# Kernel optimization log

Hardware: AMD Instinct MI355X
Metric: run time of the kernel (lower is better)

The kernel has to match this reference:

```python
import jax, jax.numpy as jnp
import numpy as np

G, N, F_IN, H, C = 128, 512, 128, 128, 10
LAMB = 1.0
NEG_SLOPE = 0.2
P_EDGE = 32.0 / N  # avg degree ~32


def setup_inputs() -> dict:
    key = jax.random.key(0)
    ks = jax.random.split(key, 12)
    x = jax.random.normal(ks[0], (G, N, F_IN), dtype=jnp.float32)
    # symmetric 0/1 adjacency without self loops (per-graph dense block)
    a = (jax.random.uniform(ks[1], (G, N, N)) < P_EDGE).astype(jnp.float32)
    adj = jnp.maximum(a, jnp.swapaxes(a, 1, 2)) * (1.0 - jnp.eye(N, dtype=jnp.float32))

    def lin(k, fi, fo):
        return (jax.random.normal(k, (fi, fo), dtype=jnp.float32) / np.float32(np.sqrt(fi)))

    return {
        "x": x, "adj": adj,
        "W1": lin(ks[2], F_IN, H), "b1": jnp.zeros((H,), jnp.float32),
        "W2": lin(ks[3], H, H), "b2": jnp.zeros((H,), jnp.float32),
        "W3": lin(ks[4], H, H), "b3": jnp.zeros((H,), jnp.float32),
        "att1_s": 0.1 * jax.random.normal(ks[5], (H,), dtype=jnp.float32),
        "att1_d": 0.1 * jax.random.normal(ks[6], (H,), dtype=jnp.float32),
        "att2_s": 0.1 * jax.random.normal(ks[7], (H,), dtype=jnp.float32),
        "att2_d": 0.1 * jax.random.normal(ks[8], (H,), dtype=jnp.float32),
        "Wl1": lin(ks[9], 2 * H, H), "bl1": jnp.zeros((H,), jnp.float32),
        "Wl2": lin(ks[10], H, H // 2), "bl2": jnp.zeros((H // 2,), jnp.float32),
        "Wl3": lin(ks[11], H // 2, C), "bl3": jnp.zeros((C,), jnp.float32),
    }


def gcn(x, adj, W, b):
    # GCNConv: D^{-1/2} (A + I) D^{-1/2} X W + b  (self-loop weight 1, edge weights in adj)
    deg = adj.sum(-1) + 1.0                              # [G, n]
    dinv = jax.lax.rsqrt(deg)
    xw = x @ W                                           # [G, n, H]
    agg = jnp.einsum('gij,gjf->gif', adj, dinv[..., None] * xw)
    return dinv[..., None] * agg + (dinv * dinv)[..., None] * xw + b


def info_score(x, adj):
    # HGP-SL node information score: row-wise L1 norm of (I - D^{-1} A) X
    deg = jnp.maximum(adj.sum(-1), 1.0)
    agg = jnp.einsum('gij,gjf->gif', adj, x) / deg[..., None]
    return jnp.sum(jnp.abs(x - agg), axis=-1)            # [G, n]


def hgpsl_pool(x, adj, att_s, att_d, k):
    # top-k node selection by information score, then structure learning:
    # dense (sample=False) path: e_ij = leaky_relu(att.[x_i||x_j]) + lamb*A_ij, softmax over j
    s = info_score(x, adj)
    _, idx = jax.lax.top_k(s, k)                         # [G, k]
    xk = jnp.take_along_axis(x, idx[..., None], axis=1)  # [G, k, H]
    g = jnp.arange(x.shape[0])[:, None, None]
    ak = adj[g, idx[:, :, None], idx[:, None, :]]        # induced adjacency [G, k, k]
    e = jax.nn.leaky_relu((xk @ att_s)[:, :, None] + (xk @ att_d)[:, None, :], NEG_SLOPE)
    attn = jax.nn.softmax(e + LAMB * ak, axis=-1)        # new learned edge weights
    return xk, attn


def readout(x):
    # gmp || gap over nodes
    return jnp.concatenate([x.max(axis=1), x.mean(axis=1)], axis=-1)


def reference(x, adj, W1, b1, W2, b2, W3, b3, att1_s, att1_d, att2_s, att2_d,
              Wl1, bl1, Wl2, bl2, Wl3, bl3):
    h = jax.nn.relu(gcn(x, adj, W1, b1))
    h, a1 = hgpsl_pool(h, adj, att1_s, att1_d, N // 2)
    x1 = readout(h)
    h = jax.nn.relu(gcn(h, a1, W2, b2))
    h, a2 = hgpsl_pool(h, a1, att2_s, att2_d, N // 4)
    x2 = readout(h)
    h = jax.nn.relu(gcn(h, a2, W3, b3))
    x3 = readout(h)
    z = jax.nn.relu(x1) + jax.nn.relu(x2) + jax.nn.relu(x3)
    z = jax.nn.relu(z @ Wl1 + bl1)
    z = jax.nn.relu(z @ Wl2 + bl2)
    return jax.nn.softmax(z @ Wl3 + bl3, axis=-1)
```

## Files before the change

### kernel.cpp

```cpp
#include <hip/hip_runtime.h>

#define Gg   128
#define N1   512
#define FH   128
#define K1   256
#define K2   128

typedef __bf16 bf16x8 __attribute__((ext_vector_type(8)));
typedef float  floatx4 __attribute__((ext_vector_type(4)));

__device__ inline float wredsum(float v) {
#pragma unroll
    for (int o = 32; o; o >>= 1) v += __shfl_xor(v, o, 64);
    return v;
}
__device__ inline float wredmax(float v) {
#pragma unroll
    for (int o = 32; o; o >>= 1) v = fmaxf(v, __shfl_xor(v, o, 64));
    return v;
}
__device__ inline unsigned short bf_rne(float x) {
    unsigned u = __float_as_uint(x);
    return (unsigned short)((u + 0x7fffu + ((u >> 16) & 1u)) >> 16);
}
__device__ __forceinline__ void gll16(const void* gsrc, void* lds) {
    __builtin_amdgcn_global_load_lds(
        (const __attribute__((address_space(1))) unsigned int*)gsrc,
        (__attribute__((address_space(3))) unsigned int*)lds, 16, 0, 0);
}

__global__ __launch_bounds__(256) void k_prep(const float* __restrict__ adj,
        float* __restrict__ dinv_gcn, float* __restrict__ dinv_info) {
    int wave = threadIdx.x >> 6, lane = threadIdx.x & 63;
    long long row = (long long)blockIdx.x * 4 + wave;
    const float* ar = adj + row * N1;
    float s = 0.f;
#pragma unroll
    for (int c = 0; c < 2; ++c) {
        float4 v = *(const float4*)(ar + lane * 8 + c * 4);
        s += (v.x + v.y) + (v.z + v.w);
    }
    s = wredsum(s);
    if (lane == 0) {
        dinv_gcn[row]  = rsqrtf(s + 1.0f);
        dinv_info[row] = 1.0f / fmaxf(s, 1.0f);
    }
}

__global__ __launch_bounds__(256) void k_tsplit(const float* __restrict__ feat,
        unsigned short* __restrict__ Thi, unsigned short* __restrict__ Tmid,
        unsigned short* __restrict__ Tlo) {
    __shared__ float tile[64 * 65];
    int b = blockIdx.x;
    int g = b >> 4, rb = (b >> 1) & 7, cb = b & 1;
    int t = threadIdx.x;
    {
        int r0 = t >> 4, c4 = t & 15;
#pragma unroll
        for (int i = 0; i < 4; ++i) {
            int r = r0 + i * 16;
            float4 v = *(const float4*)(feat + ((long long)g * 512 + rb * 64 + r) * 128 + cb * 64 + c4 * 4);
            tile[r * 65 + c4 * 4 + 0] = v.x;
            tile[r * 65 + c4 * 4 + 1] = v.y;
            tile[r * 65 + c4 * 4 + 2] = v.z;
            tile[r * 65 + c4 * 4 + 3] = v.w;
        }
    }
    __syncthreads();
    int tf = t >> 2, chunk = t & 3;
    unsigned short hbuf[16] __attribute__((aligned(16)));
    unsigned short mbuf[16] __attribute__((aligned(16)));
    unsigned short lbuf[16] __attribute__((aligned(16)));
#pragma unroll
    for (int i = 0; i < 16; ++i) {
        int m = chunk * 16 + i;
        float v = tile[m * 65 + tf];
        unsigned short h = bf_rne(v);
        float fh = __uint_as_float((unsigned)h << 16);
        float r1 = v - fh;
        unsigned short md = bf_rne(r1);
        float fm = __uint_as_float((unsigned)md << 16);
        float r2 = r1 - fm;
        unsigned short lo = bf_rne(r2);
        hbuf[i] = h; mbuf[i] = md; lbuf[i] = lo;
    }
    int f = cb * 64 + tf;
    long long obase = (long long)g * 65536 + (rb * 2 + (chunk >> 1)) * 4096
                    + f * 32 + (chunk & 1) * 16;
    *(uint4*)(Thi + obase)      = *(const uint4*)&hbuf[0];
    *(uint4*)(Thi + obase + 8)  = *(const uint4*)&hbuf[8];
    *(uint4*)(Tmid + obase)     = *(const uint4*)&mbuf[0];
    *(uint4*)(Tmid + obase + 8) = *(const uint4*)&mbuf[8];
    *(uint4*)(Tlo + obase)      = *(const uint4*)&lbuf[0];
    *(uint4*)(Tlo + obase + 8)  = *(const uint4*)&lbuf[8];
}

template<int EPI>
__global__ __launch_bounds__(256) void k_aggmm(const float* __restrict__ adjf,
        const unsigned short* __restrict__ Bhi, const unsigned short* __restrict__ Bmid,
        const unsigned short* __restrict__ Blo,
        const float* __restrict__ dvec, const float* __restrict__ hx,
        const float* __restrict__ bias, float* __restrict__ outH, float* __restrict__ outS) {
    __shared__ unsigned short Al[128 * 40];
    __shared__ unsigned short Blin[3][4096];
    __shared__ float sred[2][128];
    int b = blockIdx.x;
    int g  = (b & 7) + ((b >> 5) << 3);
    int rb = (b >> 3) & 3;
    int tid = threadIdx.x;
    int w = tid >> 6, lane = tid & 63;
    int wm = w >> 1, wn = w & 1;
    int ln = lane & 15, quad = lane >> 4;
    floatx4 acc[4][4];
#pragma unroll
    for (int i = 0; i < 4; ++i)
#pragma unroll
        for (int j = 0; j < 4; ++j) { floatx4 z = {0.f, 0.f, 0.f, 0.f}; acc[i][j] = z; }

    const char* bsrc0 = (const char*)(Bhi  + (long long)g * 65536);
    const char* bsrc1 = (const char*)(Bmid + (long long)g * 65536);
    const char* bsrc2 = (const char*)(Blo  + (long long)g * 65536);
    const long long arow0 = ((long long)g * 512 + rb * 128) * 512;
    for (int kk = 0; kk < 512; kk += 32) {
        __syncthreads();
        {
            long long soff = (long long)(kk >> 5) * 8192 + (w * 2048) + (lane << 4);
            char* l0 = (char*)&Blin[0][0] + w * 2048;
            char* l1 = (char*)&Blin[1][0] + w * 2048;
            char* l2 = (char*)&Blin[2][0] + w * 2048;
            gll16(bsrc0 + soff,        l0);
            gll16(bsrc0 + soff + 1024, l0 + 1024);
            gll16(bsrc1 + soff,        l1);
            gll16(bsrc1 + soff + 1024, l1 + 1024);
            gll16(bsrc2 + soff,        l2);
            gll16(bsrc2 + soff + 1024, l2 + 1024);
        }
#pragma unroll
        for (int i = 0; i < 4; ++i) {
            int id = tid + i * 256;
            int r = id >> 3, c = id & 7;
            float4 v = *(const float4*)(adjf + arow0 + (long long)r * 512 + kk + c * 4);
            ushort4 u;
            u.x = (unsigned short)(__float_as_uint(v.x) >> 16);
            u.y = (unsigned short)(__float_as_uint(v.y) >> 16);
            u.z = (unsigned short)(__float_as_uint(v.z) >> 16);
            u.w = (unsigned short)(__float_as_uint(v.w) >> 16);
            *(ushort4*)&Al[r * 40 + c * 4] = u;
        }
        __syncthreads();
        bf16x8 af[4];
#pragma unroll
        for (int tm = 0; tm < 4; ++tm)
            af[tm] = *(const bf16x8*)&Al[(wm * 64 + tm * 16 + ln) * 40 + quad * 8];
#pragma unroll
        for (int s = 0; s < 3; ++s) {
#pragma unroll
            for (int tn = 0; tn < 4; ++tn) {
                bf16x8 bfr = *(const bf16x8*)&Blin[s][(wn * 64 + tn * 16 + ln) * 32 + quad * 8];
#pragma unroll
                for (int tm = 0; tm < 4; ++tm)
                    acc[tm][tn] = __builtin_amdgcn_mfma_f32_16x16x32_bf16(af[tm], bfr, acc[tm][tn], 0, 0, 0);
            }
        }
    }
    long long rowbase = (long long)g * 512 + rb * 128;
    if (EPI == 0) {
#pragma unroll
        for (int tm = 0; tm < 4; ++tm)
#pragma unroll
        for (int r = 0; r < 4; ++r) {
            int ml = wm * 64 + tm * 16 + quad * 4 + r;
            long long grow = rowbase + ml;
            float di = dvec[grow];
#pragma unroll
            for (int tn = 0; tn < 4; ++tn) {
                int nc = wn * 64 + tn * 16 + ln;
                float hv = hx[grow * 128 + nc];
                float o = fmaxf(fmaf(di, acc[tm][tn][r] + hv, bias[nc]), 0.f);
                outH[grow * 128 + nc] = o;
            }
        }
    } else {
#pragma unroll
        for (int tm = 0; tm < 4; ++tm)
#pragma unroll
        for (int r = 0; r < 4; ++r) {
            int ml = wm * 64 + tm * 16 + quad * 4 + r;
            long long grow = rowbase + ml;
            float di = dvec[grow];
            float v = 0.f;
#pragma unroll
            for (int tn = 0; tn < 4; ++tn) {
                int nc = wn * 64 + tn * 16 + ln;
                float hv = hx[grow * 128 + nc];
                v += fabsf(hv - acc[tm][tn][r] * di);
            }
            v += __shfl_xor(v, 1); v += __shfl_xor(v, 2);
            v += __shfl_xor(v, 4); v += __shfl_xor(v, 8);
            if (ln == 0) sred[wn][ml] = v;
        }
        __syncthreads();
        if (tid < 128) outS[rowbase + tid] = sred[0][tid] + sred[1][tid];
    }
}

__global__ __launch_bounds__(256) void k_gemm_rw(const float* __restrict__ A,
        const float* __restrict__ W, float* __restrict__ C,
        const float* __restrict__ rs) {
    __shared__ float Al[64][68];
    __shared__ float Wl[64][132];
    long long row0 = (long long)blockIdx.x * 64;
    int tid = threadIdx.x, tr = tid >> 4, tc = tid & 15;
    float acc[4][8] = {};
    for (int ch = 0; ch < 2; ++ch) {
        for (int p = tid; p < 1024; p += 256) {
            int r = p >> 4, c4 = p & 15;
            *(float4*)&Al[r][c4 * 4] = *(const float4*)(A + (row0 + r) * 128 + ch * 64 + c4 * 4);
        }
        for (int p = tid; p < 2048; p += 256) {
            int r = p >> 5, c4 = p & 31;
            *(float4*)&Wl[r][c4 * 4] = *(const float4*)(W + (ch * 64 + r) * 128 + c4 * 4);
        }
        __syncthreads();
        for (int k = 0; k < 64; ++k) {
            float4 w0 = *(const float4*)&Wl[k][tc * 8];
            float4 w1 = *(const float4*)&Wl[k][tc * 8 + 4];
            float w[8] = {w0.x, w0.y, w0.z, w0.w, w1.x, w1.y, w1.z, w1.w};
#pragma unroll
            for (int i = 0; i < 4; ++i) {
                float a = Al[tr * 4 + i][k];
#pragma unroll
                for (int j = 0; j < 8; ++j) acc[i][j] = fmaf(a, w[j], acc[i][j]);
            }
        }
        __syncthreads();
    }
#pragma unroll
    for (int i = 0; i < 4; ++i) {
        long long r = row0 + tr * 4 + i;
        float sc = rs ? rs[r] : 1.0f;
        *(float4*)(C + r * 128 + tc * 8)     = make_float4(sc * acc[i][0], sc * acc[i][1], sc * acc[i][2], sc * acc[i][3]);
        *(float4*)(C + r * 128 + tc * 8 + 4) = make_float4(sc * acc[i][4], sc * acc[i][5], sc * acc[i][6], sc * acc[i][7]);
    }
}

template<int NT, int KSEL>
__global__ __launch_bounds__(256) void k_topk(const float* __restrict__ s, int* __restrict__ idx) {
    __shared__ unsigned long long keys[NT];
    int g = blockIdx.x;
    const float* sg = s + g * NT;
    for (int t = threadIdx.x; t < NT; t += 256) {
        unsigned int b = __float_as_uint(sg[t]);
        unsigned int ord = (b & 0x80000000u) ? ~b : (b | 0x80000000u);
        keys[t] = ((unsigned long long)(~ord) << 32) | (unsigned int)t;
    }
    __syncthreads();
    for (int k = 2; k <= NT; k <<= 1) {
        for (int j = k >> 1; j > 0; j >>= 1) {
            for (int i = threadIdx.x; i < NT; i += 256) {
                int l = i ^ j;
                if (l > i) {
                    bool dir = ((i & k) == 0);
                    unsigned long long a = keys[i], b2 = keys[l];
                    bool sw = dir ? (a > b2) : (a < b2);
                    if (sw) { keys[i] = b2; keys[l] = a; }
                }
            }
            __syncthreads();
        }
    }
    for (int t = threadIdx.x; t < KSEL; t += 256)
        idx[g * KSEL + t] = (int)(keys[t] & 0xffffffffu);
}

template<int KK>
__global__ __launch_bounds__(256) void k_gather(const float* __restrict__ h, int srcN,
        const int* __restrict__ idx, const float* __restrict__ atts, const float* __restrict__ attd,
        float* __restrict__ xk, float* __restrict__ as_, float* __restrict__ ad_) {
    int wave = threadIdx.x >> 6, lane = threadIdx.x & 63;
    int r = blockIdx.x * 4 + wave;
    int g = r / KK;
    int j = idx[r];
    float2 v = *(const float2*)(h + ((long long)g * srcN + j) * 128 + lane * 2);
    *(float2*)(xk + (long long)r * 128 + lane * 2) = v;
    float2 sv = *(const float2*)(atts + lane * 2);
    float2 dv = *(const float2*)(attd + lane * 2);
    float ps = v.x * sv.x + v.y * sv.y;
    float pd = v.x * dv.x + v.y * dv.y;
    ps = wredsum(ps); pd = wredsum(pd);
    if (lane == 0) { as_[r] = ps; ad_[r] = pd; }
}

template<int KK, int SRCN>
__global__ __launch_bounds__(256) void k_attn(const float* __restrict__ adjSrc,
        const int* __restrict__ idx, const float* __restrict__ as_, const float* __restrict__ ad_,
        float* __restrict__ attn, float* __restrict__ dgo, float* __restrict__ dio) {
    constexpr int E = KK / 64;
    __shared__ int   idxL[KK];
    __shared__ float adL[KK];
    __shared__ float rowL[4][SRCN];
    int bpg = KK / 4;
    int g = blockIdx.x / bpg;
    int wave = threadIdx.x >> 6, lane = threadIdx.x & 63;
    int i = (blockIdx.x % bpg) * 4 + wave;
    for (int t = threadIdx.x; t < KK; t += 256) { idxL[t] = idx[g * KK + t]; adL[t] = ad_[g * KK + t]; }
    __syncthreads();
    int ri = idxL[i];
    const float* arow = adjSrc + ((long long)g * SRCN + ri) * SRCN;
    for (int c = lane; c < SRCN; c += 64) rowL[wave][c] = arow[c];
    float asi = as_[g * KK + i];
    float vals[E];
    float m = -1e30f;
#pragma unroll
    for (int e = 0; e < E; ++e) {
        int j = e * 64 + lane;
        float x = asi + adL[j];
        x = (x >= 0.f) ? x : 0.2f * x;
        x += rowL[wave][idxL[j]];
        vals[e] = x; m = fmaxf(m, x);
    }
    m = wredmax(m);
    float S = 0.f;
#pragma unroll
    for (int e = 0; e < E; ++e) { vals[e] = expf(vals[e] - m); S += vals[e]; }
    S = wredsum(S);
    float inv = 1.f / S, rs = 0.f;
    float* orow = attn + ((long long)g * KK + i) * KK;
#pragma unroll
    for (int e = 0; e < E; ++e) { float p = vals[e] * inv; rs += p; orow[e * 64 + lane] = p; }
    rs = wredsum(rs);
    if (lane == 0) { dgo[g * KK + i] = rsqrtf(rs + 1.f); dio[g * KK + i] = 1.f / fmaxf(rs, 1.f); }
}

template<int KK>
__global__ __launch_bounds__(128) void k_readout(const float* __restrict__ xk, float* __restrict__ xo) {
    int g = blockIdx.x, f = threadIdx.x;
    const float* p = xk + (long long)g * KK * 128 + f;
    float m = -1e30f, s = 0.f;
    for (int r = 0; r < KK; ++r) { float v = p[r * 128]; m = fmaxf(m, v); s += v; }
    xo[g * 256 + f] = m;
    xo[g * 256 + 128 + f] = s * (1.0f / KK);
}

template<int KK, bool SCALEY, int EPI>
__global__ __launch_bounds__(256) void k_agg(const float* __restrict__ A, const float* __restrict__ Y,
        const float* __restrict__ dg, const float* __restrict__ di_,
        const float* __restrict__ bias, const float* __restrict__ hx,
        float* __restrict__ outH, float* __restrict__ outS) {
    __shared__ float Al[64][68];
    __shared__ float Yl[64][132];
    __shared__ float red[64][17];
    constexpr int RB = KK / 64;
    int g = blockIdx.x / RB;
    int rb = blockIdx.x % RB;
    const float* Ag = A + (long long)g * KK * KK;
    const float* Yg = Y + (long long)g * KK * 128;
    int tid = threadIdx.x, tr = tid >> 4, tc = tid & 15;
    float acc[4][8] = {};
    for (int ch = 0; ch < KK / 64; ++ch) {
        for (int p = tid; p < 1024; p += 256) {
            int r = p >> 4, c4 = p & 15;
            *(float4*)&Al[r][c4 * 4] = *(const float4*)(Ag + (rb * 64 + r) * KK + ch * 64 + c4 * 4);
        }
        for (int p = tid; p < 2048; p += 256) {
            int r = p >> 5, c4 = p & 31;
            float4 v = *(const float4*)(Yg + (ch * 64 + r) * 128 + c4 * 4);
            if (SCALEY) { float sc = dg[g * KK + ch * 64 + r]; v.x *= sc; v.y *= sc; v.z *= sc; v.w *= sc; }
            *(float4*)&Yl[r][c4 * 4] = v;
        }
        __syncthreads();
        for (int k = 0; k < 64; ++k) {
            float4 w0 = *(const float4*)&Yl[k][tc * 8];
            float4 w1 = *(const float4*)&Yl[k][tc * 8 + 4];
            float w[8] = {w0.x, w0.y, w0.z, w0.w, w1.x, w1.y, w1.z, w1.w};
#pragma unroll
            for (int i = 0; i < 4; ++i) {
                float a = Al[tr * 4 + i][k];
#pragma unroll
                for (int j = 0; j < 8; ++j) acc[i][j] = fmaf(a, w[j], acc[i][j]);
            }
        }
        __syncthreads();
    }
    int i0 = rb * 64 + tr * 4;
    if (EPI == 0) {
#pragma unroll
        for (int i = 0; i < 4; ++i) {
            long long gi = (long long)g * KK + i0 + i;
            float d = dg[gi], dd = d * d;
            float4 x0 = *(const float4*)(hx + gi * 128 + tc * 8);
            float4 x1 = *(const float4*)(hx + gi * 128 + tc * 8 + 4);
            float4 b0 = *(const float4*)(bias + tc * 8);
            float4 b1 = *(const float4*)(bias + tc * 8 + 4);
            float4 o0, o1;
            o0.x = fmaxf(fmaf(d, acc[i][0], fmaf(dd, x0.x, b0.x)), 0.f);
            o0.y = fmaxf(fmaf(d, acc[i][1], fmaf(dd, x0.y, b0.y)), 0.f);
            o0.z = fmaxf(fmaf(d, acc[i][2], fmaf(dd, x0.z, b0.z)), 0.f);
            o0.w = fmaxf(fmaf(d, acc[i][3], fmaf(dd, x0.w, b0.w)), 0.f);
            o1.x = fmaxf(fmaf(d, acc[i][4], fmaf(dd, x1.x, b1.x)), 0.f);
            o1.y = fmaxf(fmaf(d, acc[i][5], fmaf(dd, x1.y, b1.y)), 0.f);
            o1.z = fmaxf(fmaf(d, acc[i][6], fmaf(dd, x1.z, b1.z)), 0.f);
            o1.w = fmaxf(fmaf(d, acc[i][7], fmaf(dd, x1.w, b1.w)), 0.f);
            *(float4*)(outH + gi * 128 + tc * 8)     = o0;
            *(float4*)(outH + gi * 128 + tc * 8 + 4) = o1;
        }
    } else {
#pragma unroll
        for (int i = 0; i < 4; ++i) {
            long long gi = (long long)g * KK + i0 + i;
            float d = di_[gi];
            float4 x0 = *(const float4*)(hx + gi * 128 + tc * 8);
            float4 x1 = *(const float4*)(hx + gi * 128 + tc * 8 + 4);
            float p = fabsf(x0.x - acc[i][0] * d) + fabsf(x0.y - acc[i][1] * d)
                    + fabsf(x0.z - acc[i][2] * d) + fabsf(x0.w - acc[i][3] * d)
                    + fabsf(x1.x - acc[i][4] * d) + fabsf(x1.y - acc[i][5] * d)
                    + fabsf(x1.z - acc[i][6] * d) + fabsf(x1.w - acc[i][7] * d);
            red[tr * 4 + i][tc] = p;
        }
        __syncthreads();
        if (tid < 64) {
            float s = 0.f;
#pragma unroll
            for (int t = 0; t < 16; ++t) s += red[tid][t];
            outS[(long long)g * KK + rb * 64 + tid] = s;
        }
    }
}

__global__ __launch_bounds__(128) void k_mlp(const float* __restrict__ x1, const float* __restrict__ x2,
        const float* __restrict__ x3,
        const float* __restrict__ Wl1, const float* __restrict__ bl1,
        const float* __restrict__ Wl2, const float* __restrict__ bl2,
        const float* __restrict__ Wl3, const float* __restrict__ bl3,
        float* __restrict__ out) {
    __shared__ float z[256], z1[128], z2[64], lg[10];
    int g = blockIdx.x, t = threadIdx.x;
    for (int k = t; k < 256; k += 128)
        z[k] = fmaxf(x1[g * 256 + k], 0.f) + fmaxf(x2[g * 256 + k], 0.f) + fmaxf(x3[g * 256 + k], 0.f);
    __syncthreads();
    {
        float acc = bl1[t];
        for (int k = 0; k < 256; ++k) acc = fmaf(z[k], Wl1[k * 128 + t], acc);
        z1[t] = fmaxf(acc, 0.f);
    }
    __syncthreads();
    if (t < 64) {
        float acc = bl2[t];
        for (int k = 0; k < 128; ++k) acc = fmaf(z1[k], Wl2[k * 64 + t], acc);
        z2[t] = fmaxf(acc, 0.f);
    }
    __syncthreads();
    if (t < 10) {
        float acc = bl3[t];
        for (int k = 0; k < 64; ++k) acc = fmaf(z2[k], Wl3[k * 10 + t], acc);
        lg[t] = acc;
    }
    __syncthreads();
    if (t == 0) {
        float m = -1e30f;
        for (int c = 0; c < 10; ++c) m = fmaxf(m, lg[c]);
        float S = 0.f;
        float e[10];
        for (int c = 0; c < 10; ++c) { e[c] = expf(lg[c] - m); S += e[c]; }
        float inv = 1.f / S;
        for (int c = 0; c < 10; ++c) out[g * 10 + c] = e[c] * inv;
    }
}

extern "C" void kernel_launch(void* const* d_in, const int* in_sizes, int n_in,
                              void* d_out, int out_size, void* d_ws, size_t ws_size,
                              hipStream_t stream) {
    const float* x     = (const float*)d_in[0];
    const float* adj   = (const float*)d_in[1];
    const float* W1    = (const float*)d_in[2];
    const float* b1    = (const float*)d_in[3];
    const float* W2    = (const float*)d_in[4];
    const float* b2    = (const float*)d_in[5];
    const float* W3    = (const float*)d_in[6];
    const float* b3    = (const float*)d_in[7];
    const float* att1s = (const float*)d_in[8];
    const float* att1d = (const float*)d_in[9];
    const float* att2s = (const float*)d_in[10];
    const float* att2d = (const float*)d_in[11];
    const float* Wl1   = (const float*)d_in[12];
    const float* bl1   = (const float*)d_in[13];
    const float* Wl2   = (const float*)d_in[14];
    const float* bl2   = (const float*)d_in[15];
    const float* Wl3   = (const float*)d_in[16];
    const float* bl3   = (const float*)d_in[17];
    float* out = (float*)d_out;

    char* ws = (char*)d_ws;
    unsigned short* Thi  = (unsigned short*)(ws + 0);
    unsigned short* Tmid = (unsigned short*)(ws + 16777216);
    unsigned short* Tlo  = (unsigned short*)(ws + 33554432);
    float* xk1 = (float*)(ws + 0);
    float* xw2 = (float*)(ws + 16777216);
    float* h2  = (float*)(ws + 33554432);
    float* xk2 = (float*)(ws + 16777216);
    float* a2  = (float*)(ws + 25165824);
    float* xw3 = (float*)(ws + 0);
    float* h3  = (float*)(ws + 8388608);
    float* dxw1 = (float*)(ws + 50331648);
    float* h1   = dxw1;
    float* a1   = dxw1;
    float* s1      = (float*)(ws + 83886080);
    int*   idx1    = (int*)  (ws + 84148224);
    float* as1     = (float*)(ws + 84279296);
    float* ad1     = (float*)(ws + 84410368);
    float* dinv_g1 = (float*)(ws + 84541440);
    float* dinv_i1 = (float*)(ws + 84803584);
    float* dinv_g2 = (float*)(ws + 85065728);
    float* dinv_i2 = (float*)(ws + 85196800);
    float* x1r     = (float*)(ws + 85327872);
    float* s2      = (float*)(ws + 85458944);
    int*   idx2    = (int*)  (ws + 85590016);
    float* as2     = (float*)(ws + 85655552);
    float* ad2     = (float*)(ws + 85721088);
    float* dinv_g3 = (float*)(ws + 85786624);
    float* dinv_i3 = (float*)(ws + 85852160);
    float* x2r     = (float*)(ws + 85917696);
    float* x3r     = (float*)(ws + 86048768);

    k_prep<<<Gg * N1 / 4, 256, 0, stream>>>(adj, dinv_g1, dinv_i1);
    k_gemm_rw<<<Gg * N1 / 64, 256, 0, stream>>>(x, W1, dxw1, dinv_g1);
    k_tsplit<<<Gg * 16, 256, 0, stream>>>(dxw1, Thi, Tmid, Tlo);
    k_aggmm<0><<<Gg * 4, 256, 0, stream>>>(adj, Thi, Tmid, Tlo, dinv_g1, dxw1, b1, h1, nullptr);
    k_tsplit<<<Gg * 16, 256, 0, stream>>>(h1, Thi, Tmid, Tlo);
    k_aggmm<1><<<Gg * 4, 256, 0, stream>>>(adj, Thi, Tmid, Tlo, dinv_i1, h1, nullptr, nullptr, s1);
    k_topk<N1, K1><<<Gg, 256, 0, stream>>>(s1, idx1);
    k_gather<K1><<<Gg * K1 / 4, 256, 0, stream>>>(h1, N1, idx1, att1s, att1d, xk1, as1, ad1);
    k_readout<K1><<<Gg, 128, 0, stream>>>(xk1, x1r);
    k_attn<K1, N1><<<Gg * K1 / 4, 256, 0, stream>>>(adj, idx1, as1, ad1, a1, dinv_g2, dinv_i2);

    k_gemm_rw<<<Gg * K1 / 64, 256, 0, stream>>>(xk1, W2, xw2, nullptr);
    k_agg<K1, true, 0><<<Gg * (K1 / 64), 256, 0, stream>>>(a1, xw2, dinv_g2, dinv_i2, b2, xw2, h2, nullptr);
    k_agg<K1, false, 1><<<Gg * (K1 / 64), 256, 0, stream>>>(a1, h2, dinv_g2, dinv_i2, b2, h2, nullptr, s2);
    k_topk<K1, K2><<<Gg, 256, 0, stream>>>(s2, idx2);
    k_gather<K2><<<Gg * K2 / 4, 256, 0, stream>>>(h2, K1, idx2, att2s, att2d, xk2, as2, ad2);
    k_readout<K2><<<Gg, 128, 0, stream>>>(xk2, x2r);
    k_attn<K2, K1><<<Gg * K2 / 4, 256, 0, stream>>>(a1, idx2, as2, ad2, a2, dinv_g3, dinv_i3);

    k_gemm_rw<<<Gg * K2 / 64, 256, 0, stream>>>(xk2, W3, xw3, nullptr);
    k_agg<K2, true, 0><<<Gg * (K2 / 64), 256, 0, stream>>>(a2, xw3, dinv_g3, dinv_i3, b3, xw3, h3, nullptr);
    k_readout<K2><<<Gg, 128, 0, stream>>>(h3, x3r);

    k_mlp<<<Gg, 128, 0, stream>>>(x1r, x2r, x3r, Wl1, bl1, Wl2, bl2, Wl3, bl3, out);
}
```

Baseline: 599.3 us.

## Pre-convert adjacency to bf16 once and stream it via async LDS loads with XOR swizzle

k_prep now writes a bf16 copy of the adjacency while it computes degrees. Both k_aggmm launches then read this half-size copy with global_load_lds instead of reading fp32 rows and converting them in registers. The A and B LDS tiles use an XOR-swizzled 64-byte row layout, and k_tsplit writes its output pre-swizzled to match, so fragment reads avoid bank conflicts without padding. This cuts adjacency traffic in the two big aggregation passes and removes the per-tile conversion. In exchange it adds one extra bf16 write of the full adjacency and relies on the workspace being large enough at the new offset.

Measured after the change: 607.6 us. No clear change (+1.4%).

```diff
diff --git a/kernel.cpp b/kernel.cpp
--- a/kernel.cpp
+++ b/kernel.cpp
@@ -30,16 +30,23 @@
 }
 
 __global__ __launch_bounds__(256) void k_prep(const float* __restrict__ adj,
+        unsigned short* __restrict__ adjbf,
         float* __restrict__ dinv_gcn, float* __restrict__ dinv_info) {
     int wave = threadIdx.x >> 6, lane = threadIdx.x & 63;
     long long row = (long long)blockIdx.x * 4 + wave;
     const float* ar = adj + row * N1;
     float s = 0.f;
+    unsigned short ub[8] __attribute__((aligned(16)));
 #pragma unroll
     for (int c = 0; c < 2; ++c) {
         float4 v = *(const float4*)(ar + lane * 8 + c * 4);
         s += (v.x + v.y) + (v.z + v.w);
-    }
+        ub[c * 4 + 0] = (unsigned short)(__float_as_uint(v.x) >> 16);
+        ub[c * 4 + 1] = (unsigned short)(__float_as_uint(v.y) >> 16);
+        ub[c * 4 + 2] = (unsigned short)(__float_as_uint(v.z) >> 16);
+        ub[c * 4 + 3] = (unsigned short)(__float_as_uint(v.w) >> 16);
+    }
+    *(uint4*)(adjbf + row * N1 + lane * 8) = *(const uint4*)ub;
     s = wredsum(s);
     if (lane == 0) {
         dinv_gcn[row]  = rsqrtf(s + 1.0f);
@@ -84,24 +91,26 @@
         unsigned short lo = bf_rne(r2);
         hbuf[i] = h; mbuf[i] = md; lbuf[i] = lo;
     }
-    int f = cb * 64 + tf;
+    int sxz = (tf >> 1) & 3;
+    int c0 = (chunk & 1) * 2;
+    int p0 = (c0 ^ sxz) * 8, p1 = ((c0 + 1) ^ sxz) * 8;
     long long obase = (long long)g * 65536 + (rb * 2 + (chunk >> 1)) * 4096
-                    + f * 32 + (chunk & 1) * 16;
-    *(uint4*)(Thi + obase)      = *(const uint4*)&hbuf[0];
-    *(uint4*)(Thi + obase + 8)  = *(const uint4*)&hbuf[8];
-    *(uint4*)(Tmid + obase)     = *(const uint4*)&mbuf[0];
-    *(uint4*)(Tmid + obase + 8) = *(const uint4*)&mbuf[8];
-    *(uint4*)(Tlo + obase)      = *(const uint4*)&lbuf[0];
-    *(uint4*)(Tlo + obase + 8)  = *(const uint4*)&lbuf[8];
+                    + (cb * 64 + tf) * 32;
+    *(uint4*)(Thi + obase + p0)  = *(const uint4*)&hbuf[0];
+    *(uint4*)(Thi + obase + p1)  = *(const uint4*)&hbuf[8];
+    *(uint4*)(Tmid + obase + p0) = *(const uint4*)&mbuf[0];
+    *(uint4*)(Tmid + obase + p1) = *(const uint4*)&mbuf[8];
+    *(uint4*)(Tlo + obase + p0)  = *(const uint4*)&lbuf[0];
+    *(uint4*)(Tlo + obase + p1)  = *(const uint4*)&lbuf[8];
 }
 
 template<int EPI>
-__global__ __launch_bounds__(256) void k_aggmm(const float* __restrict__ adjf,
+__global__ __launch_bounds__(256) void k_aggmm(const unsigned short* __restrict__ adjbf,
         const unsigned short* __restrict__ Bhi, const unsigned short* __restrict__ Bmid,
         const unsigned short* __restrict__ Blo,
         const float* __restrict__ dvec, const float* __restrict__ hx,
         const float* __restrict__ bias, float* __restrict__ outH, float* __restrict__ outS) {
-    __shared__ unsigned short Al[128 * 40];
+    __shared__ unsigned short Al[4096];
     __shared__ unsigned short Blin[3][4096];
     __shared__ float sred[2][128];
     int b = blockIdx.x;
@@ -111,6 +120,7 @@
     int w = tid >> 6, lane = tid & 63;
     int wm = w >> 1, wn = w & 1;
     int ln = lane & 15, quad = lane >> 4;
+    int aoff = ((quad ^ ((lane >> 1) & 3)) << 4);
     floatx4 acc[4][4];
 #pragma unroll
     for (int i = 0; i < 4; ++i)
@@ -120,9 +130,19 @@
     const char* bsrc0 = (const char*)(Bhi  + (long long)g * 65536);
     const char* bsrc1 = (const char*)(Bmid + (long long)g * 65536);
     const char* bsrc2 = (const char*)(Blo  + (long long)g * 65536);
-    const long long arow0 = ((long long)g * 512 + rb * 128) * 512;
+    int r1 = w * 32 + (lane >> 2);
+    int c1 = (lane & 3) ^ ((r1 >> 1) & 3);
+    int r2 = r1 + 16;
+    int c2 = (lane & 3) ^ ((r2 >> 1) & 3);
+    const unsigned short* abase = adjbf + ((long long)g * 512 + rb * 128) * 512;
+    const unsigned short* asrc1 = abase + (long long)r1 * 512 + c1 * 8;
+    const unsigned short* asrc2 = abase + (long long)r2 * 512 + c2 * 8;
+    char* aldst = (char*)Al + w * 2048;
+
     for (int kk = 0; kk < 512; kk += 32) {
         __syncthreads();
+        gll16(asrc1 + kk, aldst);
+        gll16(asrc2 + kk, aldst + 1024);
         {
             long long soff = (long long)(kk >> 5) * 8192 + (w * 2048) + (lane << 4);
             char* l0 = (char*)&Blin[0][0] + w * 2048;
@@ -135,28 +155,17 @@
             gll16(bsrc2 + soff,        l2);
             gll16(bsrc2 + soff + 1024, l2 + 1024);
         }
-#pragma unroll
-        for (int i = 0; i < 4; ++i) {
-            int id = tid + i * 256;
-            int r = id >> 3, c = id & 7;
-            float4 v = *(const float4*)(adjf + arow0 + (long long)r * 512 + kk + c * 4);
-            ushort4 u;
-            u.x = (unsigned short)(__float_as_uint(v.x) >> 16);
-            u.y = (unsigned short)(__float_as_uint(v.y) >> 16);
-            u.z = (unsigned short)(__float_as_uint(v.z) >> 16);
-            u.w = (unsigned short)(__float_as_uint(v.w) >> 16);
-            *(ushort4*)&Al[r * 40 + c * 4] = u;
-        }
         __syncthreads();
         bf16x8 af[4];
 #pragma unroll
         for (int tm = 0; tm < 4; ++tm)
-            af[tm] = *(const bf16x8*)&Al[(wm * 64 + tm * 16 + ln) * 40 + quad * 8];
+            af[tm] = *(const bf16x8*)((const char*)Al + (wm * 64 + tm * 16 + ln) * 64 + aoff);
 #pragma unroll
         for (int s = 0; s < 3; ++s) {
 #pragma unroll
             for (int tn = 0; tn < 4; ++tn) {
-                bf16x8 bfr = *(const bf16x8*)&Blin[s][(wn * 64 + tn * 16 + ln) * 32 + quad * 8];
+                bf16x8 bfr = *(const bf16x8*)((const char*)&Blin[s][0]
+                                              + (wn * 64 + tn * 16 + ln) * 64 + aoff);
 #pragma unroll
                 for (int tm = 0; tm < 4; ++tm)
                     acc[tm][tn] = __builtin_amdgcn_mfma_f32_16x16x32_bf16(af[tm], bfr, acc[tm][tn], 0, 0, 0);
@@ -521,13 +530,14 @@
     float* dinv_i3 = (float*)(ws + 85852160);
     float* x2r     = (float*)(ws + 85917696);
     float* x3r     = (float*)(ws + 86048768);
-
-    k_prep<<<Gg * N1 / 4, 256, 0, stream>>>(adj, dinv_g1, dinv_i1);
+    unsigned short* adjbf = (unsigned short*)(ws + 100663296);
+
+    k_prep<<<Gg * N1 / 4, 256, 0, stream>>>(adj, adjbf, dinv_g1, dinv_i1);
     k_gemm_rw<<<Gg * N1 / 64, 256, 0, stream>>>(x, W1, dxw1, dinv_g1);
     k_tsplit<<<Gg * 16, 256, 0, stream>>>(dxw1, Thi, Tmid, Tlo);
-    k_aggmm<0><<<Gg * 4, 256, 0, stream>>>(adj, Thi, Tmid, Tlo, dinv_g1, dxw1, b1, h1, nullptr);
+    k_aggmm<0><<<Gg * 4, 256, 0, stream>>>(adjbf, Thi, Tmid, Tlo, dinv_g1, dxw1, b1, h1, nullptr);
     k_tsplit<<<Gg * 16, 256, 0, stream>>>(h1, Thi, Tmid, Tlo);
-    k_aggmm<1><<<Gg * 4, 256, 0, stream>>>(adj, Thi, Tmid, Tlo, dinv_i1, h1, nullptr, nullptr, s1);
+    k_aggmm<1><<<Gg * 4, 256, 0, stream>>>(adjbf, Thi, Tmid, Tlo, dinv_i1, h1, nullptr, nullptr, s1);
     k_topk<N1, K1><<<Gg, 256, 0, stream>>>(s1, idx1);
     k_gather<K1><<<Gg * K1 / 4, 256, 0, stream>>>(h1, N1, idx1, att1s, att1d, xk1, as1, ad1);
     k_readout<K1><<<Gg, 128, 0, stream>>>(xk1, x1r);
```
